# Kernel tuning notes

Measured on AMD Instinct MI355X. Metric: run time of the kernel, lower is better.

Reference implementation:

```python
import jax, jax.numpy as jnp
import numpy as np

DIM = 1024
NUM_HEADS = 16
HEAD_DIM = DIM // NUM_HEADS
SCALE = HEAD_DIM ** -0.5


def rotate_half(x):
    x1, x2 = jnp.split(x, 2, axis=-1)
    return jnp.concatenate((-x2, x1), axis=-1)


def setup_inputs() -> dict:
    key = jax.random.key(0)
    ks = jax.random.split(key, 8)
    B, N = 2, 2048
    x = jax.random.normal(ks[0], (B, N, DIM), dtype=jnp.float32)
    # RoPE tables, broadcast over batch and heads
    pos = jnp.arange(N, dtype=jnp.float32)[:, None]
    inv_freq = 1.0 / (10000.0 ** (jnp.arange(0, HEAD_DIM, 2, dtype=jnp.float32) / HEAD_DIM))
    ang = pos * inv_freq[None, :]                       # [N, HEAD_DIM/2]
    ang = jnp.concatenate([ang, ang], axis=-1)          # [N, HEAD_DIM]
    rope_cos = jnp.cos(ang)[None, None]                 # [1,1,N,HEAD_DIM]
    rope_sin = jnp.sin(ang)[None, None]
    s = DIM ** -0.5
    qkv_w = jax.random.normal(ks[1], (3 * DIM, DIM), dtype=jnp.float32) * s
    qkv_b = jnp.zeros((3 * DIM,), dtype=jnp.float32)
    proj_w = jax.random.normal(ks[2], (DIM, DIM), dtype=jnp.float32) * s
    proj_b = jnp.zeros((DIM,), dtype=jnp.float32)
    return {"x": x, "rope_cos": rope_cos, "rope_sin": rope_sin,
            "qkv_w": qkv_w, "qkv_b": qkv_b, "proj_w": proj_w, "proj_b": proj_b}


def reference(x, rope_cos, rope_sin, qkv_w, qkv_b, proj_w, proj_b):
    B, N, C = x.shape
    H, D = NUM_HEADS, HEAD_DIM
    qkv = x @ qkv_w.T + qkv_b                            # [B,N,3C]
    qkv = qkv.reshape(B, N, 3, H, D).transpose(2, 0, 3, 1, 4)  # [3,B,H,N,D]
    q, k, v = qkv[0], qkv[1], qkv[2]
    # RoPE on q, k
    q = q * rope_cos + rotate_half(q) * rope_sin
    k = k * rope_cos + rotate_half(k) * rope_sin
    # scaled dot-product attention
    scores = jnp.einsum('bhnd,bhmd->bhnm', q, k) * SCALE
    attn = jax.nn.softmax(scores, axis=-1)
    out = jnp.einsum('bhnm,bhmd->bhnd', attn, v)         # [B,H,N,D]
    out = out.transpose(0, 2, 1, 3).reshape(B, N, C)
    return out @ proj_w.T + proj_b
```

## Files before the change

### kernel.cpp

```cpp
#include <hip/hip_runtime.h>
#include <hip/hip_bf16.h>

#define NUM_HEADS 16
#define HEAD_DIM 64
#define DIM 1024
#define NTOK 2048
#define MTOT 4096

typedef __attribute__((ext_vector_type(8))) short bf16x8;
typedef __attribute__((ext_vector_type(4))) float f32x4;
typedef __attribute__((ext_vector_type(16))) float f32x16;
typedef __attribute__((ext_vector_type(2))) unsigned int uint2v;

__device__ __forceinline__ unsigned short f2bf(float f) {
    union { __hip_bfloat16 h; unsigned short u; } c;
    c.h = __float2bfloat16(f);
    return c.u;
}

__device__ __forceinline__ unsigned int packbf(float lo, float hi) {
    union { unsigned short us[2]; unsigned int u; } p;
    p.us[0] = f2bf(lo); p.us[1] = f2bf(hi);
    return p.u;
}

__device__ __forceinline__ void plswap(unsigned int &a, unsigned int &b) {
#if __has_builtin(__builtin_amdgcn_permlane32_swap)
    uint2v r = __builtin_amdgcn_permlane32_swap(a, b, false, false);
    a = r[0]; b = r[1];
#else
    unsigned int pa = (unsigned int)__shfl_xor((int)a, 32);
    unsigned int pb = (unsigned int)__shfl_xor((int)b, 32);
    bool hi = (threadIdx.x & 32) != 0;
    unsigned int an = hi ? pb : a;
    unsigned int bn = hi ? b : pa;
    a = an; b = bn;
#endif
}

__device__ __forceinline__ void gload16(const unsigned short* g, unsigned short* l) {
    __builtin_amdgcn_global_load_lds(
        (const __attribute__((address_space(1))) void*)g,
        (__attribute__((address_space(3))) void*)l, 16, 0, 0);
}

__global__ __launch_bounds__(256) void k_conv3(
    const float* __restrict__ s0, unsigned short* __restrict__ d0, int n0,
    const float* __restrict__ s1, unsigned short* __restrict__ d1, int n1,
    const float* __restrict__ s2, unsigned short* __restrict__ d2, int n2)
{
    int blk = blockIdx.x;
    int b0 = n0 >> 11, b1 = n1 >> 11;
    const float* s; unsigned short* d; int i;
    if (blk < b0)            { s = s0; d = d0; i = blk; }
    else if (blk < b0 + b1)  { s = s1; d = d1; i = blk - b0; }
    else                     { s = s2; d = d2; i = blk - b0 - b1; }
    int idx = (i * 256 + threadIdx.x) * 8;
    float4 a = *(const float4*)(s + idx);
    float4 b = *(const float4*)(s + idx + 4);
    union { unsigned short us[8]; uint4 u4; } p;
    p.us[0] = f2bf(a.x); p.us[1] = f2bf(a.y); p.us[2] = f2bf(a.z); p.us[3] = f2bf(a.w);
    p.us[4] = f2bf(b.x); p.us[5] = f2bf(b.y); p.us[6] = f2bf(b.z); p.us[7] = f2bf(b.w);
    *(uint4*)(d + idx) = p.u4;
}

__global__ __launch_bounds__(256) void k_gemm_qkv(
    const unsigned short* __restrict__ xb, const unsigned short* __restrict__ wb,
    const float* __restrict__ bias, const float* __restrict__ rcos,
    const float* __restrict__ rsin,
    unsigned short* __restrict__ qb, unsigned short* __restrict__ kb,
    unsigned short* __restrict__ vtb)
{
    __shared__ __align__(16) unsigned char smem[34816];
    unsigned short* As = (unsigned short*)smem;
    unsigned short* Bs = (unsigned short*)(smem + 16384);

    const int tid  = threadIdx.x;
    const int lane = tid & 63;
    const int wid  = tid >> 6;
    const int lr   = lane & 15;
    const int g    = lane >> 4;
    const int wm   = (wid >> 1) * 64;
    const int wn   = (wid & 1) * 64;
    const int m0   = blockIdx.y * 128;
    const int n0   = blockIdx.x * 128;

    f32x4 acc[4][4];
    #pragma unroll
    for (int i = 0; i < 4; ++i)
        #pragma unroll
        for (int j = 0; j < 4; ++j) acc[i][j] = (f32x4){0.f, 0.f, 0.f, 0.f};

    for (int k0 = 0; k0 < DIM; k0 += 64) {
        #pragma unroll
        for (int it = 0; it < 4; ++it) {
            int p   = tid + it * 256;
            int row = p >> 3;
            int c   = (p & 7) ^ (row & 7);
            gload16(xb + (size_t)(m0 + row) * DIM + k0 + c*8, As + p*8);
            gload16(wb + (size_t)(n0 + row) * DIM + k0 + c*8, Bs + p*8);
        }
        __syncthreads();
        #pragma unroll
        for (int kk = 0; kk < 2; ++kk) {
            bf16x8 af[4], bfr[4];
            #pragma unroll
            for (int i = 0; i < 4; ++i) {
                int row = wm + i*16 + lr;
                af[i] = *(const bf16x8*)(As + row*64 + (((kk*4 + g) ^ (row & 7)) << 3));
            }
            #pragma unroll
            for (int j = 0; j < 4; ++j) {
                int row = wn + j*16 + lr;
                bfr[j] = *(const bf16x8*)(Bs + row*64 + (((kk*4 + g) ^ (row & 7)) << 3));
            }
            #pragma unroll
            for (int i = 0; i < 4; ++i)
                #pragma unroll
                for (int j = 0; j < 4; ++j)
                    acc[i][j] = __builtin_amdgcn_mfma_f32_16x16x32_bf16(af[i], bfr[j], acc[i][j], 0, 0, 0);
        }
        __syncthreads();
    }

    const int sect = n0 >> 10;
    float bq[4];
    #pragma unroll
    for (int j = 0; j < 4; ++j) bq[j] = bias[n0 + wn + j*16 + lr];

    if (sect < 2) {
        unsigned short* dst = sect ? kb : qb;
        const float sc = sect ? 1.0f : 0.125f * 1.44269504088896f;
        const int h = ((n0 & 1023) + wn) >> 6;
        #pragma unroll
        for (int i = 0; i < 4; ++i) {
            #pragma unroll
            for (int v = 0; v < 4; ++v) {
                int gm = m0 + wm + i*16 + g*4 + v;
                int b  = gm >> 11, n = gm & 2047;
                size_t base = ((size_t)(b*NUM_HEADS + h) * NTOK + n) << 6;
                #pragma unroll
                for (int j = 0; j < 4; ++j) {
                    int d = j*16 + lr;
                    float val = acc[i][j][v] + bq[j];
                    float vp  = acc[i][j^2][v] + bq[j^2];
                    float rot = (j < 2) ? -vp : vp;
                    float c = rcos[n*64 + d], s = rsin[n*64 + d];
                    dst[base + d] = f2bf((val * c + rot * s) * sc);
                }
            }
        }
    } else {
        unsigned short (*vt)[136] = (unsigned short (*)[136])smem;
        __syncthreads();
        #pragma unroll
        for (int i = 0; i < 4; ++i)
            #pragma unroll
            for (int j = 0; j < 4; ++j)
                #pragma unroll
                for (int v = 0; v < 4; ++v) {
                    int row = wm + i*16 + g*4 + v;
                    int c   = wn + j*16 + lr;
                    vt[c][row] = f2bf(acc[i][j][v] + bq[j]);
                }
        __syncthreads();
        const int b = m0 >> 11;
        const int nbase = m0 & 2047;
        #pragma unroll
        for (int it = 0; it < 8; ++it) {
            int c   = (tid >> 4) + it * 16;
            int sc2 = (n0 & 1023) + c;
            int hh  = sc2 >> 6, d = sc2 & 63;
            int nloc = (tid & 15) * 8;
            uint4 val = *(uint4*)&vt[c][nloc];
            *(uint4*)(vtb + ((size_t)(b*NUM_HEADS + hh) * HEAD_DIM + d) * NTOK + nbase + nloc) = val;
        }
    }
}

__global__ __launch_bounds__(256, 2) void k_attn(
    const unsigned short* __restrict__ qb, const unsigned short* __restrict__ kb,
    const unsigned short* __restrict__ vtb, unsigned short* __restrict__ attnb)
{
    __shared__ __align__(16) char sb[65536];

    const int tid  = threadIdx.x;
    const int lane = tid & 63;
    const int w    = tid >> 6;
    const int hi   = lane >> 5;
    const int lc   = lane & 31;
    const int qg   = w >> 1;
    const int kvg  = w & 1;
    const int q0   = blockIdx.y * 128;
    const int bh   = blockIdx.x;
    const int b    = bh >> 4, h = bh & 15;

    int koff[2][4];
    #pragma unroll
    for (int s = 0; s < 2; ++s)
        #pragma unroll
        for (int ks = 0; ks < 4; ++ks)
            koff[s][ks] = (64*kvg + 32*s + lc) * 128 + (((2*ks + hi) ^ (lc & 7)) << 4);
    int voff[2][4];
    #pragma unroll
    for (int dt = 0; dt < 2; ++dt)
        #pragma unroll
        for (int c4 = 0; c4 < 4; ++c4)
            voff[dt][c4] = 32768 + (32*dt + lc) * 256 + (((8*kvg + 2*c4 + hi) ^ (lc & 15)) << 4);

    const unsigned short* gk[4];
    const unsigned short* gv[4];
    char* dk[4]; char* dv[4];
    {
        const unsigned short* kbase = kb  + (size_t)bh * NTOK * 64;
        const unsigned short* vbase = vtb + (size_t)bh * HEAD_DIM * NTOK;
        #pragma unroll
        for (int it = 0; it < 4; ++it) {
            int p  = tid + it * 256;
            int kr = p >> 3;
            int kc = (p & 7) ^ (kr & 7);
            gk[it] = kbase + kr*64 + kc*8;
            dk[it] = sb + p*16;
            int vr = p >> 4;
            int vc = (p & 15) ^ (vr & 15);
            gv[it] = vbase + (size_t)vr*NTOK + vc*8;
            dv[it] = sb + 32768 + p*16;
        }
    }

    bf16x8 qa[2][4];
    #pragma unroll
    for (int qt = 0; qt < 2; ++qt) {
        size_t qrow = ((size_t)bh * NTOK + q0 + 64*qg + 32*qt + lc) * 64;
        #pragma unroll
        for (int ks = 0; ks < 4; ++ks)
            qa[qt][ks] = *(const bf16x8*)(qb + qrow + ks*16 + hi*8);
    }

    const f32x16 z16 = {0.f,0.f,0.f,0.f, 0.f,0.f,0.f,0.f, 0.f,0.f,0.f,0.f, 0.f,0.f,0.f,0.f};
    f32x16 o2[2][2];
    o2[0][0] = z16; o2[0][1] = z16; o2[1][0] = z16; o2[1][1] = z16;
    float lsum0 = 0.f, lsum1 = 0.f;

    #pragma unroll
    for (int it = 0; it < 4; ++it) {
        gload16(gk[it], (unsigned short*)dk[it]);
        gload16(gv[it], (unsigned short*)dv[it]);
        gk[it] += 8192; gv[it] += 128;
    }
    __syncthreads();

#define SUM16(SS) ( (((SS[0]+SS[1])+(SS[2]+SS[3])) + ((SS[4]+SS[5])+(SS[6]+SS[7]))) + \
                    (((SS[8]+SS[9])+(SS[10]+SS[11])) + ((SS[12]+SS[13])+(SS[14]+SS[15]))) )

#define PACKQT(SS, PB0, PB1)                                                     \
    {                                                                            \
        _Pragma("unroll")                                                        \
        for (int u = 0; u < 2; ++u) {                                            \
            unsigned int a0 = packbf(SS[8*u],     SS[8*u + 1]);                  \
            unsigned int b0 = packbf(SS[8*u + 4], SS[8*u + 5]);                  \
            unsigned int a1 = packbf(SS[8*u + 2], SS[8*u + 3]);                  \
            unsigned int b1 = packbf(SS[8*u + 6], SS[8*u + 7]);                  \
            plswap(a0, b0);                                                      \
            plswap(a1, b1);                                                      \
            union { unsigned int u4[4]; bf16x8 v; } pk;                          \
            pk.u4[0] = a0; pk.u4[1] = a1; pk.u4[2] = b0; pk.u4[3] = b1;          \
            if (u == 0) (PB0) = pk.v; else (PB1) = pk.v;                         \
        }                                                                        \
    }

#define ATTN_ITER(X, DO_STAGE)                                                   \
    {                                                                            \
        if (DO_STAGE) {                                                          \
            _Pragma("unroll")                                                    \
            for (int it = 0; it < 4; ++it) {                                     \
                gload16(gk[it], (unsigned short*)(dk[it] + ((X) ^ 16384)));      \
                gload16(gv[it], (unsigned short*)(dv[it] + ((X) ^ 16384)));      \
                gk[it] += 8192; gv[it] += 128;                                   \
            }                                                                    \
        }                                                                        \
        _Pragma("unroll")                                                        \
        for (int s = 0; s < 2; ++s) {                                            \
            bf16x8 kf[4];                                                        \
            _Pragma("unroll")                                                    \
            for (int ks = 0; ks < 4; ++ks)                                       \
                kf[ks] = *(const bf16x8*)(sb + (X) + koff[s][ks]);               \
            __builtin_amdgcn_s_setprio(1);                                       \
            f32x16 S0 = __builtin_amdgcn_mfma_f32_32x32x16_bf16(kf[0], qa[0][0], z16, 0, 0, 0); \
            f32x16 S1 = __builtin_amdgcn_mfma_f32_32x32x16_bf16(kf[0], qa[1][0], z16, 0, 0, 0); \
            _Pragma("unroll")                                                    \
            for (int ks = 1; ks < 4; ++ks) {                                     \
                S0 = __builtin_amdgcn_mfma_f32_32x32x16_bf16(kf[ks], qa[0][ks], S0, 0, 0, 0); \
                S1 = __builtin_amdgcn_mfma_f32_32x32x16_bf16(kf[ks], qa[1][ks], S1, 0, 0, 0); \
            }                                                                    \
            __builtin_amdgcn_s_setprio(0);                                       \
            _Pragma("unroll")                                                    \
            for (int r = 0; r < 16; ++r) {                                       \
                S0[r] = __builtin_amdgcn_exp2f(S0[r]);                           \
                S1[r] = __builtin_amdgcn_exp2f(S1[r]);                           \
            }                                                                    \
            lsum0 += SUM16(S0);                                                  \
            lsum1 += SUM16(S1);                                                  \
            bf16x8 p00, p01, p10, p11;                                           \
            PACKQT(S0, p00, p01);                                                \
            PACKQT(S1, p10, p11);                                                \
            _Pragma("unroll")                                                    \
            for (int u = 0; u < 2; ++u) {                                        \
                bf16x8 pb0 = u ? p01 : p00;                                      \
                bf16x8 pb1 = u ? p11 : p10;                                      \
                _Pragma("unroll")                                                \
                for (int dt = 0; dt < 2; ++dt) {                                 \
                    bf16x8 vf = *(const bf16x8*)(sb + (X) + voff[dt][2*s + u]);  \
                    __builtin_amdgcn_s_setprio(1);                               \
                    o2[0][dt] = __builtin_amdgcn_mfma_f32_32x32x16_bf16(vf, pb0, o2[0][dt], 0, 0, 0); \
                    o2[1][dt] = __builtin_amdgcn_mfma_f32_32x32x16_bf16(vf, pb1, o2[1][dt], 0, 0, 0); \
                    __builtin_amdgcn_s_setprio(0);                               \
                }                                                                \
            }                                                                    \
        }                                                                        \
        __syncthreads();                                                         \
    }

    #pragma unroll 1
    for (int tt = 0; tt < NTOK/128; tt += 2) {
        ATTN_ITER(0,     true);
        ATTN_ITER(16384, (tt + 2 < NTOK/128));
    }
#undef ATTN_ITER
#undef PACKQT
#undef SUM16

    lsum0 += __shfl_xor(lsum0, 32);
    lsum1 += __shfl_xor(lsum1, 32);

    if (kvg == 1) {
        char* base = sb + qg * 16384;
        #pragma unroll
        for (int qt = 0; qt < 2; ++qt)
            #pragma unroll
            for (int dt = 0; dt < 2; ++dt)
                #pragma unroll
                for (int part = 0; part < 4; ++part) {
                    f32x4 v4;
                    #pragma unroll
                    for (int v = 0; v < 4; ++v) v4[v] = o2[qt][dt][part*4 + v];
                    *(f32x4*)(base + ((qt*2 + dt)*4 + part)*1024 + lane*16) = v4;
                }
        *(float*)(sb + 32768 + (qg*2 + 0)*256 + lane*4) = lsum0;
        *(float*)(sb + 32768 + (qg*2 + 1)*256 + lane*4) = lsum1;
    }
    __syncthreads();
    if (kvg == 0) {
        char* base = sb + qg * 16384;
        float lp0 = *(const float*)(sb + 32768 + (qg*2 + 0)*256 + lane*4);
        float lp1 = *(const float*)(sb + 32768 + (qg*2 + 1)*256 + lane*4);
        const float inv0 = 1.0f / (lsum0 + lp0);
        const float inv1 = 1.0f / (lsum1 + lp1);
        #pragma unroll
        for (int qt = 0; qt < 2; ++qt) {
            const float inv = qt ? inv1 : inv0;
            int q = q0 + 64*qg + 32*qt + lc;
            size_t obase = ((size_t)(b*NTOK + q)) * DIM + h*HEAD_DIM;
            #pragma unroll
            for (int dt = 0; dt < 2; ++dt)
                #pragma unroll
                for (int c = 0; c < 4; ++c) {
                    f32x4 vp = *(const f32x4*)(base + ((qt*2 + dt)*4 + c)*1024 + lane*16);
                    union { unsigned short us[4]; uint2 u2; } pk4;
                    #pragma unroll
                    for (int v = 0; v < 4; ++v)
                        pk4.us[v] = f2bf((o2[qt][dt][c*4 + v] + vp[v]) * inv);
                    *(uint2*)(attnb + obase + dt*32 + 8*c + 4*hi) = pk4.u2;
                }
        }
    }
}

__global__ __launch_bounds__(256) void k_proj(
    const unsigned short* __restrict__ a, const unsigned short* __restrict__ wb,
    const float* __restrict__ bias, float* __restrict__ out)
{
    __shared__ __align__(16) unsigned short As[8192];
    __shared__ __align__(16) unsigned short Bs[4096];

    const int tid  = threadIdx.x;
    const int lane = tid & 63;
    const int wid  = tid >> 6;
    const int lr   = lane & 15;
    const int g    = lane >> 4;
    const int wm   = (wid & 1) * 64;
    const int wn   = (wid >> 1) * 32;
    const int m0   = blockIdx.y * 128;
    const int n0   = blockIdx.x * 64;

    f32x4 acc[4][2];
    #pragma unroll
    for (int i = 0; i < 4; ++i)
        #pragma unroll
        for (int j = 0; j < 2; ++j) acc[i][j] = (f32x4){0.f, 0.f, 0.f, 0.f};

    for (int k0 = 0; k0 < DIM; k0 += 64) {
        #pragma unroll
        for (int it = 0; it < 4; ++it) {
            int p   = tid + it * 256;
            int row = p >> 3;
            int c   = (p & 7) ^ (row & 7);
            gload16(a + (size_t)(m0 + row) * DIM + k0 + c*8, As + p*8);
        }
        #pragma unroll
        for (int it = 0; it < 2; ++it) {
            int p   = tid + it * 256;
            int row = p >> 3;
            int c   = (p & 7) ^ (row & 7);
            gload16(wb + (size_t)(n0 + row) * DIM + k0 + c*8, Bs + p*8);
        }
        __syncthreads();
        #pragma unroll
        for (int kk = 0; kk < 2; ++kk) {
            bf16x8 af[4], bfr[2];
            #pragma unroll
            for (int i = 0; i < 4; ++i) {
                int row = wm + i*16 + lr;
                af[i] = *(const bf16x8*)(As + row*64 + (((kk*4 + g) ^ (row & 7)) << 3));
            }
            #pragma unroll
            for (int j = 0; j < 2; ++j) {
                int row = wn + j*16 + lr;
                bfr[j] = *(const bf16x8*)(Bs + row*64 + (((kk*4 + g) ^ (row & 7)) << 3));
            }
            #pragma unroll
            for (int i = 0; i < 4; ++i)
                #pragma unroll
                for (int j = 0; j < 2; ++j)
                    acc[i][j] = __builtin_amdgcn_mfma_f32_16x16x32_bf16(af[i], bfr[j], acc[i][j], 0, 0, 0);
        }
        __syncthreads();
    }

    #pragma unroll
    for (int i = 0; i < 4; ++i)
        #pragma unroll
        for (int j = 0; j < 2; ++j)
            #pragma unroll
            for (int v = 0; v < 4; ++v) {
                int row = m0 + wm + i*16 + g*4 + v;
                int col = n0 + wn + j*16 + lr;
                out[(size_t)row * DIM + col] = acc[i][j][v] + bias[col];
            }
}

extern "C" void kernel_launch(void* const* d_in, const int* in_sizes, int n_in,
                              void* d_out, int out_size, void* d_ws, size_t ws_size,
                              hipStream_t stream)
{
    const float* x      = (const float*)d_in[0];
    const float* rcos   = (const float*)d_in[1];
    const float* rsin   = (const float*)d_in[2];
    const float* qkv_w  = (const float*)d_in[3];
    const float* qkv_b  = (const float*)d_in[4];
    const float* proj_w = (const float*)d_in[5];
    const float* proj_b = (const float*)d_in[6];
    float* out = (float*)d_out;

    const size_t BUF = (size_t)2 * NUM_HEADS * NTOK * HEAD_DIM;
    unsigned short* qb    = (unsigned short*)d_ws;
    unsigned short* kb    = qb + BUF;
    unsigned short* vtb   = kb + BUF;
    unsigned short* attnb = vtb + BUF;
    unsigned short* xbf   = attnb + BUF;
    unsigned short* wqkvb = xbf + (size_t)MTOT * DIM;
    unsigned short* wprjb = wqkvb + (size_t)3 * DIM * DIM;

    const int n0 = MTOT * DIM, n1 = 3 * DIM * DIM, n2 = DIM * DIM;
    k_conv3<<<dim3((n0 + n1 + n2) / 2048), 256, 0, stream>>>(
        x, xbf, n0, qkv_w, wqkvb, n1, proj_w, wprjb, n2);

    k_gemm_qkv<<<dim3(24, 32), 256, 0, stream>>>(xbf, wqkvb, qkv_b, rcos, rsin, qb, kb, vtb);
    k_attn<<<dim3(32, NTOK/128), 256, 0, stream>>>(qb, kb, vtb, attnb);
    k_proj<<<dim3(16, 32), 256, 0, stream>>>(attnb, wprjb, proj_b, out);
}
```

Baseline: 116.5 us.

## Switch GEMMs to 32x32 MFMA and compute softmax row sums via MFMA

The QKV and projection GEMMs now use 32x32x16 bf16 MFMA tiles instead of 16x16x32, which cuts LDS fragment loads per FLOP and changes the accumulator layout and epilogue indexing. In attention, the per-lane scalar SUM16 reductions of softmax probabilities are replaced by extra MFMAs against a ones vector, which moves that reduction from VALU onto the matrix cores and removes a cross-lane shuffle. The V-fragment loads are hoisted and the MFMAs regrouped. The cost is four extra MFMAs per iteration, and the row sums now come from bf16-rounded probabilities, which slightly changes numerics.

```diff
diff --git a/kernel.cpp b/kernel.cpp
--- a/kernel.cpp
+++ b/kernel.cpp
@@ -78,18 +78,16 @@
     const int tid  = threadIdx.x;
     const int lane = tid & 63;
     const int wid  = tid >> 6;
-    const int lr   = lane & 15;
-    const int g    = lane >> 4;
+    const int lc   = lane & 31;
+    const int hi   = lane >> 5;
     const int wm   = (wid >> 1) * 64;
     const int wn   = (wid & 1) * 64;
     const int m0   = blockIdx.y * 128;
     const int n0   = blockIdx.x * 128;
 
-    f32x4 acc[4][4];
-    #pragma unroll
-    for (int i = 0; i < 4; ++i)
-        #pragma unroll
-        for (int j = 0; j < 4; ++j) acc[i][j] = (f32x4){0.f, 0.f, 0.f, 0.f};
+    const f32x16 z16 = {0.f,0.f,0.f,0.f, 0.f,0.f,0.f,0.f, 0.f,0.f,0.f,0.f, 0.f,0.f,0.f,0.f};
+    f32x16 acc[2][2];
+    acc[0][0] = z16; acc[0][1] = z16; acc[1][0] = z16; acc[1][1] = z16;
 
     for (int k0 = 0; k0 < DIM; k0 += 64) {
         #pragma unroll
@@ -102,49 +100,49 @@
         }
         __syncthreads();
         #pragma unroll
-        for (int kk = 0; kk < 2; ++kk) {
-            bf16x8 af[4], bfr[4];
-            #pragma unroll
-            for (int i = 0; i < 4; ++i) {
-                int row = wm + i*16 + lr;
-                af[i] = *(const bf16x8*)(As + row*64 + (((kk*4 + g) ^ (row & 7)) << 3));
+        for (int kk = 0; kk < 4; ++kk) {
+            bf16x8 af[2], bfr[2];
+            #pragma unroll
+            for (int i = 0; i < 2; ++i) {
+                int row = wm + i*32 + lc;
+                af[i] = *(const bf16x8*)(As + row*64 + (((kk*2 + hi) ^ (row & 7)) << 3));
             }
             #pragma unroll
-            for (int j = 0; j < 4; ++j) {
-                int row = wn + j*16 + lr;
-                bfr[j] = *(const bf16x8*)(Bs + row*64 + (((kk*4 + g) ^ (row & 7)) << 3));
+            for (int j = 0; j < 2; ++j) {
+                int row = wn + j*32 + lc;
+                bfr[j] = *(const bf16x8*)(Bs + row*64 + (((kk*2 + hi) ^ (row & 7)) << 3));
             }
             #pragma unroll
-            for (int i = 0; i < 4; ++i)
+            for (int i = 0; i < 2; ++i)
                 #pragma unroll
-                for (int j = 0; j < 4; ++j)
-                    acc[i][j] = __builtin_amdgcn_mfma_f32_16x16x32_bf16(af[i], bfr[j], acc[i][j], 0, 0, 0);
+                for (int j = 0; j < 2; ++j)
+                    acc[i][j] = __builtin_amdgcn_mfma_f32_32x32x16_bf16(af[i], bfr[j], acc[i][j], 0, 0, 0);
         }
         __syncthreads();
     }
 
     const int sect = n0 >> 10;
-    float bq[4];
-    #pragma unroll
-    for (int j = 0; j < 4; ++j) bq[j] = bias[n0 + wn + j*16 + lr];
+    float bq[2];
+    #pragma unroll
+    for (int j = 0; j < 2; ++j) bq[j] = bias[n0 + wn + j*32 + lc];
 
     if (sect < 2) {
         unsigned short* dst = sect ? kb : qb;
         const float sc = sect ? 1.0f : 0.125f * 1.44269504088896f;
         const int h = ((n0 & 1023) + wn) >> 6;
         #pragma unroll
-        for (int i = 0; i < 4; ++i) {
-            #pragma unroll
-            for (int v = 0; v < 4; ++v) {
-                int gm = m0 + wm + i*16 + g*4 + v;
+        for (int i = 0; i < 2; ++i) {
+            #pragma unroll
+            for (int r = 0; r < 16; ++r) {
+                int gm = m0 + wm + i*32 + (r & 3) + 8*(r >> 2) + 4*hi;
                 int b  = gm >> 11, n = gm & 2047;
                 size_t base = ((size_t)(b*NUM_HEADS + h) * NTOK + n) << 6;
                 #pragma unroll
-                for (int j = 0; j < 4; ++j) {
-                    int d = j*16 + lr;
-                    float val = acc[i][j][v] + bq[j];
-                    float vp  = acc[i][j^2][v] + bq[j^2];
-                    float rot = (j < 2) ? -vp : vp;
+                for (int j = 0; j < 2; ++j) {
+                    int d = j*32 + lc;
+                    float val = acc[i][j][r] + bq[j];
+                    float vp  = acc[i][j^1][r] + bq[j^1];
+                    float rot = (j == 0) ? -vp : vp;
                     float c = rcos[n*64 + d], s = rsin[n*64 + d];
                     dst[base + d] = f2bf((val * c + rot * s) * sc);
                 }
@@ -154,14 +152,14 @@
         unsigned short (*vt)[136] = (unsigned short (*)[136])smem;
         __syncthreads();
         #pragma unroll
-        for (int i = 0; i < 4; ++i)
-            #pragma unroll
-            for (int j = 0; j < 4; ++j)
+        for (int i = 0; i < 2; ++i)
+            #pragma unroll
+            for (int j = 0; j < 2; ++j)
                 #pragma unroll
-                for (int v = 0; v < 4; ++v) {
-                    int row = wm + i*16 + g*4 + v;
-                    int c   = wn + j*16 + lr;
-                    vt[c][row] = f2bf(acc[i][j][v] + bq[j]);
+                for (int r = 0; r < 16; ++r) {
+                    int row = wm + i*32 + (r & 3) + 8*(r >> 2) + 4*hi;
+                    int c   = wn + j*32 + lc;
+                    vt[c][row] = f2bf(acc[i][j][r] + bq[j]);
                 }
         __syncthreads();
         const int b = m0 >> 11;
@@ -238,9 +236,13 @@
     }
 
     const f32x16 z16 = {0.f,0.f,0.f,0.f, 0.f,0.f,0.f,0.f, 0.f,0.f,0.f,0.f, 0.f,0.f,0.f,0.f};
+    bf16x8 onesa;
+    #pragma unroll
+    for (int j = 0; j < 8; ++j) onesa[j] = (short)0x3F80;
+
     f32x16 o2[2][2];
     o2[0][0] = z16; o2[0][1] = z16; o2[1][0] = z16; o2[1][1] = z16;
-    float lsum0 = 0.f, lsum1 = 0.f;
+    f32x16 ol0 = z16, ol1 = z16;
 
     #pragma unroll
     for (int it = 0; it < 4; ++it) {
@@ -249,9 +251,6 @@
         gk[it] += 8192; gv[it] += 128;
     }
     __syncthreads();
-
-#define SUM16(SS) ( (((SS[0]+SS[1])+(SS[2]+SS[3])) + ((SS[4]+SS[5])+(SS[6]+SS[7]))) + \
-                    (((SS[8]+SS[9])+(SS[10]+SS[11])) + ((SS[12]+SS[13])+(SS[14]+SS[15]))) )
 
 #define PACKQT(SS, PB0, PB1)                                                     \
     {                                                                            \
@@ -299,24 +298,27 @@
                 S0[r] = __builtin_amdgcn_exp2f(S0[r]);                           \
                 S1[r] = __builtin_amdgcn_exp2f(S1[r]);                           \
             }                                                                    \
-            lsum0 += SUM16(S0);                                                  \
-            lsum1 += SUM16(S1);                                                  \
             bf16x8 p00, p01, p10, p11;                                           \
             PACKQT(S0, p00, p01);                                                \
             PACKQT(S1, p10, p11);                                                \
-            _Pragma("unroll")                                                    \
-            for (int u = 0; u < 2; ++u) {                                        \
-                bf16x8 pb0 = u ? p01 : p00;                                      \
-                bf16x8 pb1 = u ? p11 : p10;                                      \
-                _Pragma("unroll")                                                \
-                for (int dt = 0; dt < 2; ++dt) {                                 \
-                    bf16x8 vf = *(const bf16x8*)(sb + (X) + voff[dt][2*s + u]);  \
-                    __builtin_amdgcn_s_setprio(1);                               \
-                    o2[0][dt] = __builtin_amdgcn_mfma_f32_32x32x16_bf16(vf, pb0, o2[0][dt], 0, 0, 0); \
-                    o2[1][dt] = __builtin_amdgcn_mfma_f32_32x32x16_bf16(vf, pb1, o2[1][dt], 0, 0, 0); \
-                    __builtin_amdgcn_s_setprio(0);                               \
-                }                                                                \
-            }                                                                    \
+            bf16x8 vf00 = *(const bf16x8*)(sb + (X) + voff[0][2*s + 0]);         \
+            bf16x8 vf10 = *(const bf16x8*)(sb + (X) + voff[1][2*s + 0]);         \
+            bf16x8 vf01 = *(const bf16x8*)(sb + (X) + voff[0][2*s + 1]);         \
+            bf16x8 vf11 = *(const bf16x8*)(sb + (X) + voff[1][2*s + 1]);         \
+            __builtin_amdgcn_s_setprio(1);                                       \
+            o2[0][0] = __builtin_amdgcn_mfma_f32_32x32x16_bf16(vf00, p00, o2[0][0], 0, 0, 0); \
+            o2[0][1] = __builtin_amdgcn_mfma_f32_32x32x16_bf16(vf10, p00, o2[0][1], 0, 0, 0); \
+            o2[1][0] = __builtin_amdgcn_mfma_f32_32x32x16_bf16(vf00, p10, o2[1][0], 0, 0, 0); \
+            o2[1][1] = __builtin_amdgcn_mfma_f32_32x32x16_bf16(vf10, p10, o2[1][1], 0, 0, 0); \
+            o2[0][0] = __builtin_amdgcn_mfma_f32_32x32x16_bf16(vf01, p01, o2[0][0], 0, 0, 0); \
+            o2[0][1] = __builtin_amdgcn_mfma_f32_32x32x16_bf16(vf11, p01, o2[0][1], 0, 0, 0); \
+            o2[1][0] = __builtin_amdgcn_mfma_f32_32x32x16_bf16(vf01, p11, o2[1][0], 0, 0, 0); \
+            o2[1][1] = __builtin_amdgcn_mfma_f32_32x32x16_bf16(vf11, p11, o2[1][1], 0, 0, 0); \
+            ol0 = __builtin_amdgcn_mfma_f32_32x32x16_bf16(onesa, p00, ol0, 0, 0, 0); \
+            ol0 = __builtin_amdgcn_mfma_f32_32x32x16_bf16(onesa, p01, ol0, 0, 0, 0); \
+            ol1 = __builtin_amdgcn_mfma_f32_32x32x16_bf16(onesa, p10, ol1, 0, 0, 0); \
+            ol1 = __builtin_amdgcn_mfma_f32_32x32x16_bf16(onesa, p11, ol1, 0, 0, 0); \
+            __builtin_amdgcn_s_setprio(0);                                       \
         }                                                                        \
         __syncthreads();                                                         \
     }
@@ -328,10 +330,9 @@
     }
 #undef ATTN_ITER
 #undef PACKQT
-#undef SUM16
-
-    lsum0 += __shfl_xor(lsum0, 32);
-    lsum1 += __shfl_xor(lsum1, 32);
+
+    float lsum0 = ol0[0];
+    float lsum1 = ol1[0];
 
     if (kvg == 1) {
         char* base = sb + qg * 16384;
@@ -386,18 +387,16 @@
     const int tid  = threadIdx.x;
     const int lane = tid & 63;
     const int wid  = tid >> 6;
-    const int lr   = lane & 15;
-    const int g    = lane >> 4;
+    const int lc   = lane & 31;
+    const int hi   = lane >> 5;
     const int wm   = (wid & 1) * 64;
     const int wn   = (wid >> 1) * 32;
     const int m0   = blockIdx.y * 128;
     const int n0   = blockIdx.x * 64;
 
-    f32x4 acc[4][2];
-    #pragma unroll
-    for (int i = 0; i < 4; ++i)
-        #pragma unroll
-        for (int j = 0; j < 2; ++j) acc[i][j] = (f32x4){0.f, 0.f, 0.f, 0.f};
+    const f32x16 z16 = {0.f,0.f,0.f,0.f, 0.f,0.f,0.f,0.f, 0.f,0.f,0.f,0.f, 0.f,0.f,0.f,0.f};
+    f32x16 acc[2];
+    acc[0] = z16; acc[1] = z16;
 
     for (int k0 = 0; k0 < DIM; k0 += 64) {
         #pragma unroll
@@ -416,37 +415,32 @@
         }
         __syncthreads();
         #pragma unroll
-        for (int kk = 0; kk < 2; ++kk) {
-            bf16x8 af[4], bfr[2];
-            #pragma unroll
-            for (int i = 0; i < 4; ++i) {
-                int row = wm + i*16 + lr;
-                af[i] = *(const bf16x8*)(As + row*64 + (((kk*4 + g) ^ (row & 7)) << 3));
+        for (int kk = 0; kk < 4; ++kk) {
+            bf16x8 af[2], bf;
+            #pragma unroll
+            for (int i = 0; i < 2; ++i) {
+                int row = wm + i*32 + lc;
+                af[i] = *(const bf16x8*)(As + row*64 + (((kk*2 + hi) ^ (row & 7)) << 3));
             }
-            #pragma unroll
-            for (int j = 0; j < 2; ++j) {
-                int row = wn + j*16 + lr;
-                bfr[j] = *(const bf16x8*)(Bs + row*64 + (((kk*4 + g) ^ (row & 7)) << 3));
+            {
+                int row = wn + lc;
+                bf = *(const bf16x8*)(Bs + row*64 + (((kk*2 + hi) ^ (row & 7)) << 3));
             }
             #pragma unroll
-            for (int i = 0; i < 4; ++i)
-                #pragma unroll
-                for (int j = 0; j < 2; ++j)
-                    acc[i][j] = __builtin_amdgcn_mfma_f32_16x16x32_bf16(af[i], bfr[j], acc[i][j], 0, 0, 0);
-        }
-        __syncthreads();
-    }
-
-    #pragma unroll
-    for (int i = 0; i < 4; ++i)
-        #pragma unroll
-        for (int j = 0; j < 2; ++j)
-            #pragma unroll
-            for (int v = 0; v < 4; ++v) {
-                int row = m0 + wm + i*16 + g*4 + v;
-                int col = n0 + wn + j*16 + lr;
-                out[(size_t)row * DIM + col] = acc[i][j][v] + bias[col];
-            }
+            for (int i = 0; i < 2; ++i)
+                acc[i] = __builtin_amdgcn_mfma_f32_32x32x16_bf16(af[i], bf, acc[i], 0, 0, 0);
+        }
+        __syncthreads();
+    }
+
+    #pragma unroll
+    for (int i = 0; i < 2; ++i)
+        #pragma unroll
+        for (int r = 0; r < 16; ++r) {
+            int row = m0 + wm + i*32 + (r & 3) + 8*(r >> 2) + 4*hi;
+            int col = n0 + wn + lc;
+            out[(size_t)row * DIM + col] = acc[i][r] + bias[col];
+        }
 }
 
 extern "C" void kernel_launch(void* const* d_in, const int* in_sizes, int n_in,
```

Result: no change. 117.3 us (+0.7%).
